# Kernel optimization log

Measured on AMD Instinct MI355X. Metric: run time of the kernel, lower is better.

## Reference

```python
import jax, jax.numpy as jnp
import numpy as np

B, S, D_MODEL, H, N_LAYERS = 4, 1024, 512, 8, 6
DEPTH = D_MODEL // H


def setup_inputs() -> dict:
    key = jax.random.key(0)
    ks = jax.random.split(key, 16)
    sc = 1.0 / np.sqrt(D_MODEL)
    inp = {
        'v': jax.random.normal(ks[0], (B, S, D_MODEL), jnp.float32),
        'q': jax.random.normal(ks[1], (B, S, D_MODEL), jnp.float32),
        'k': jax.random.normal(ks[2], (B, S, D_MODEL), jnp.float32),
        'wq_w': jax.random.normal(ks[3], (D_MODEL, D_MODEL), jnp.float32) * sc,
        'wq_b': jnp.zeros((D_MODEL,), jnp.float32),
        'wk_w': jax.random.normal(ks[4], (D_MODEL, D_MODEL), jnp.float32) * sc,
        'wk_b': jnp.zeros((D_MODEL,), jnp.float32),
        'wv_w': jax.random.normal(ks[5], (D_MODEL, D_MODEL), jnp.float32) * sc,
        'wv_b': jnp.zeros((D_MODEL,), jnp.float32),
        'wo_w': jax.random.normal(ks[6], (D_MODEL, D_MODEL), jnp.float32) * sc,
        'wo_b': jnp.zeros((D_MODEL,), jnp.float32),
        'aug_hb': jax.random.uniform(ks[7], (N_LAYERS, 1), jnp.float32),
        'aug_pi': jax.random.uniform(ks[8], (N_LAYERS, 1), jnp.float32),
        'aug_at': jax.random.uniform(ks[9], (N_LAYERS, 1), jnp.float32),
        'table_hb': jax.random.normal(ks[10], (S, S), jnp.float32),
        'table_pi': jax.random.normal(ks[11], (S, S), jnp.float32),
        'mask': (jax.random.uniform(ks[12], (B, 1, S, S)) < 0.1).astype(jnp.float32),
        'block_num': 0,
    }
    return inp


def _split_heads(x):
    # (B, S, d_model) -> (B, H, S, depth)
    return x.reshape(B, S, H, DEPTH).transpose(0, 2, 1, 3)


def reference(v, q, k, wq_w, wq_b, wk_w, wk_b, wv_w, wv_b, wo_w, wo_b,
              aug_hb, aug_pi, aug_at, table_hb, table_pi, mask, block_num):
    qh = _split_heads(q @ wq_w + wq_b)
    kh = _split_heads(k @ wk_w + wk_b)
    vh = _split_heads(v @ wv_w + wv_b)

    # NOTE: original call site swaps q/k positionally, so scores = K . Q^T
    scores = jnp.einsum('bhid,bhjd->bhij', kh, qh)  # (B,H,S,S)
    dk = jnp.float32(DEPTH)
    logits = scores / jnp.sqrt(dk) + mask * (-1e9)

    # per-layer table augmentation (tables broadcast over batch & heads)
    logits = logits * aug_at[block_num] \
        + aug_hb[block_num] * table_hb \
        + aug_pi[block_num] * table_pi

    # joint softmax over axes (2, 3)
    m = jnp.max(logits, axis=(2, 3), keepdims=True)
    e = jnp.exp(logits - m)
    attn = e / jnp.sum(e, axis=(2, 3), keepdims=True)

    ctx = jnp.einsum('bhij,bhjd->bhid', attn, vh)          # (B,H,S,depth)
    ctx = ctx.transpose(0, 2, 1, 3).reshape(B, S, D_MODEL)  # concat heads
    out = ctx @ wo_w + wo_b
    return out, attn
```

## Files before the change

kernel.cpp:

```cpp
#include <hip/hip_runtime.h>
#include <math.h>

#define NS 1024
#define DM 512
#define NH 8
#define DEPTH 64

#define OFF_QH   0
#define OFF_KH   2097152
#define OFF_VH   4194304
#define OFF_CTX0 0
#define OFF_CTX1 2097152
#define OFF_PART 6291456

#define SW3(row, col) ((col) ^ ((((row) >> 3) & 3) << 3))
#define ESW(row, col) ((col) ^ ((((row) >> 3) & 7) << 2))

#define LO_SCALE 2048.0f
#define LO_INV   (1.0f/2048.0f)
#define F16_MIN_NORM 6.1035156e-5f
#define ASCALE   4096.0f
#define AUNSCALE (1.0f/4096.0f)

typedef float f4 __attribute__((ext_vector_type(4)));
typedef _Float16 h8 __attribute__((ext_vector_type(8)));
typedef float f32x4v __attribute__((ext_vector_type(4)));

#define SPLIT1(x, hi_e, lo_e) {                                          \
    const float x_ = (x);                                                \
    _Float16 t = (fabsf(x_) >= F16_MIN_NORM) ? (_Float16)x_ : (_Float16)0.f; \
    hi_e = t;                                                            \
    lo_e = (_Float16)((x_ - (float)t) * LO_SCALE);                       \
}

#define SPLIT8(u0, u1, hi, lo) {                                         \
    SPLIT1(u0.x, hi[0], lo[0]) SPLIT1(u0.y, hi[1], lo[1])                \
    SPLIT1(u0.z, hi[2], lo[2]) SPLIT1(u0.w, hi[3], lo[3])                \
    SPLIT1(u1.x, hi[4], lo[4]) SPLIT1(u1.y, hi[5], lo[5])                \
    SPLIT1(u1.z, hi[6], lo[6]) SPLIT1(u1.w, hi[7], lo[7])                \
}

#define MM(accH, accM, a_h, a_l, b_h, b_l) {                                   \
    accH = __builtin_amdgcn_mfma_f32_16x16x32_f16(a_h, b_h, accH, 0, 0, 0);    \
    accM = __builtin_amdgcn_mfma_f32_16x16x32_f16(a_l, b_h, accM, 0, 0, 0);    \
    accM = __builtin_amdgcn_mfma_f32_16x16x32_f16(a_h, b_l, accM, 0, 0, 0);    \
}

__device__ __forceinline__ void prep_one(
    const float* __restrict__ W, _Float16* __restrict__ whi,
    _Float16* __restrict__ wlo, int g)
{
    const int kk = g >> 7;
    const int n  = (g & 127) * 4;
    const float4 f = *(const float4*)(W + (size_t)kk * DM + n);
    const int gbase = (kk >> 3) * 128 + (kk & 7);
    #define PREP1(val, nn) {                                             \
        const int a_ = ((nn) >> 4) * 8192 + gbase + ((nn) & 15) * 8;     \
        _Float16 h_; _Float16 l_;                                        \
        SPLIT1(val, h_, l_)                                              \
        whi[a_] = h_; wlo[a_] = l_;                                      \
    }
    PREP1(f.x, n + 0) PREP1(f.y, n + 1) PREP1(f.z, n + 2) PREP1(f.w, n + 3)
    #undef PREP1
}

__global__ __launch_bounds__(256) void k_prep_qkv(
    const float* __restrict__ wq, const float* __restrict__ wk,
    const float* __restrict__ wv, float* __restrict__ attn)
{
    const int w = blockIdx.y;
    const float* W = (w == 0) ? wq : (w == 1) ? wk : wv;
    _Float16* base = (_Float16*)attn + (size_t)w * 524288;
    prep_one(W, base, base + 262144, blockIdx.x * 256 + threadIdx.x);
}

__global__ __launch_bounds__(256) void k_prep_wo(
    const float* __restrict__ wo, float* __restrict__ ws)
{
    _Float16* base = (_Float16*)(ws + OFF_VH);
    prep_one(wo, base, base + 262144, blockIdx.x * 256 + threadIdx.x);
}

__global__ __launch_bounds__(256, 3) void k_proj(
    const float* __restrict__ q, const float* __restrict__ k, const float* __restrict__ v,
    const float* __restrict__ bq, const float* __restrict__ bk, const float* __restrict__ bv,
    float* __restrict__ ws, const float* __restrict__ attn)
{
    const float *X, *bias; float* out; int wsel;
    if (blockIdx.z == 0)      { X=q; bias=bq; out=ws+OFF_QH; wsel=0; }
    else if (blockIdx.z == 1) { X=k; bias=bk; out=ws+OFF_KH; wsel=1; }
    else                      { X=v; bias=bv; out=ws+OFF_VH; wsel=2; }

    const int f = blockIdx.x + (blockIdx.y << 3);
    const int n0 = (f >> 5) * 64, m0 = (f & 31) * 128;
    const int tid = threadIdx.x, l = tid & 63, w = tid >> 6;
    const int lr = l & 15, lg = l >> 4;

    const _Float16* whi = (const _Float16*)attn + (size_t)wsel * 524288;
    const _Float16* wlo = whi + 262144;
    const float* ap0 = X + (size_t)(m0 + w*32 + lr) * DM + lg*8;
    const float* ap1 = ap0 + (size_t)16 * DM;
    const _Float16* bh_base = whi + (size_t)(n0 >> 4) * 8192 + lg*128 + lr*8;
    const _Float16* bl_base = wlo + (size_t)(n0 >> 4) * 8192 + lg*128 + lr*8;

    f32x4v aH00 = 0, aH01 = 0, aH02 = 0, aH03 = 0;
    f32x4v aH10 = 0, aH11 = 0, aH12 = 0, aH13 = 0;
    f32x4v aM00 = 0, aM01 = 0, aM02 = 0, aM03 = 0;
    f32x4v aM10 = 0, aM11 = 0, aM12 = 0, aM13 = 0;

    #pragma unroll 1
    for (int kb = 0; kb < DM; kb += 32) {
        h8 ah0, al0, ah1, al1;
        {
            const float4 u0 = *(const float4*)(ap0 + kb);
            const float4 u1 = *(const float4*)(ap0 + kb + 4);
            SPLIT8(u0, u1, ah0, al0);
            const float4 v0 = *(const float4*)(ap1 + kb);
            const float4 v1 = *(const float4*)(ap1 + kb + 4);
            SPLIT8(v0, v1, ah1, al1);
        }
        const int boff = kb * 16;
        const h8 bh0 = *(const h8*)(bh_base + boff);
        const h8 bh1 = *(const h8*)(bh_base + boff + 8192);
        const h8 bh2 = *(const h8*)(bh_base + boff + 16384);
        const h8 bh3 = *(const h8*)(bh_base + boff + 24576);
        const h8 bl0 = *(const h8*)(bl_base + boff);
        const h8 bl1 = *(const h8*)(bl_base + boff + 8192);
        const h8 bl2 = *(const h8*)(bl_base + boff + 16384);
        const h8 bl3 = *(const h8*)(bl_base + boff + 24576);

        MM(aH00, aM00, ah0, al0, bh0, bl0) MM(aH01, aM01, ah0, al0, bh1, bl1)
        MM(aH02, aM02, ah0, al0, bh2, bl2) MM(aH03, aM03, ah0, al0, bh3, bl3)
        MM(aH10, aM10, ah1, al1, bh0, bl0) MM(aH11, aM11, ah1, al1, bh1, bl1)
        MM(aH12, aM12, ah1, al1, bh2, bl2) MM(aH13, aM13, ah1, al1, bh3, bl3)
    }

    const int h = n0 >> 6;
    #define STORE_TILE(accH, accM, nt, mt) {                                 \
        const int n = n0 + (nt)*16 + lr;                                     \
        const float bsv = bias[n];                                           \
        const int d = n & 63;                                                \
        const int mbase = m0 + w*32 + (mt)*16 + lg*4;                        \
        _Pragma("unroll")                                                    \
        for (int r = 0; r < 4; ++r) {                                        \
            const int m = mbase + r;                                         \
            const int bb = m >> 10, s = m & 1023;                            \
            out[(((size_t)(bb*NH + h))*NS + s)*DEPTH + d] =                  \
                fmaf(accM[r], LO_INV, accH[r]) + bsv;                        \
        }                                                                    \
    }
    STORE_TILE(aH00, aM00, 0, 0) STORE_TILE(aH10, aM10, 0, 1)
    STORE_TILE(aH01, aM01, 1, 0) STORE_TILE(aH11, aM11, 1, 1)
    STORE_TILE(aH02, aM02, 2, 0) STORE_TILE(aH12, aM12, 2, 1)
    STORE_TILE(aH03, aM03, 3, 0) STORE_TILE(aH13, aM13, 3, 1)
    #undef STORE_TILE
}

__global__ __launch_bounds__(256, 4) void k_sumexp(
    float* __restrict__ ws,
    const float* __restrict__ t_hb, const float* __restrict__ t_pi,
    const float* __restrict__ mask,
    const float* __restrict__ aug_hb, const float* __restrict__ aug_pi,
    const float* __restrict__ aug_at, const int* __restrict__ bnum,
    float* __restrict__ attn)
{
    __shared__ float Ks[32][132];
    __shared__ float Qs[32][132];
    __shared__ float wred[4];
    const int bh = blockIdx.z, b = bh >> 3;
    const int f = blockIdx.x + (blockIdx.y << 3);
    const int r = f & 7, qq = f >> 3;
    const int it = ((r & 1) << 2) | (qq & 3);
    const int jt = ((r >> 1) << 1) | (qq >> 2);
    const int i0 = it * 128, j0 = jt * 128;
    const float* kh = ws + OFF_KH + (size_t)bh*NS*DEPTH;
    const float* qh = ws + OFF_QH + (size_t)bh*NS*DEPTH;
    const int tid = threadIdx.x, tx = tid & 15, ty = tid >> 4;
    const int ar_ = tid >> 3, ac4 = tid & 7;

    float acc[8][8] = {};
    for (int d0 = 0; d0 < DEPTH; d0 += 32) {
        #pragma unroll
        for (int l = 0; l < 4; ++l) {
            const int rr = ar_ + l*32;
            const float4 fk = *(const float4*)(kh + (size_t)(i0+rr)*DEPTH + d0 + ac4*4);
            Ks[ac4*4+0][SW3(ac4*4+0, rr)]=fk.x; Ks[ac4*4+1][SW3(ac4*4+1, rr)]=fk.y;
            Ks[ac4*4+2][SW3(ac4*4+2, rr)]=fk.z; Ks[ac4*4+3][SW3(ac4*4+3, rr)]=fk.w;
            const float4 fq = *(const float4*)(qh + (size_t)(j0+rr)*DEPTH + d0 + ac4*4);
            Qs[ac4*4+0][SW3(ac4*4+0, rr)]=fq.x; Qs[ac4*4+1][SW3(ac4*4+1, rr)]=fq.y;
            Qs[ac4*4+2][SW3(ac4*4+2, rr)]=fq.z; Qs[ac4*4+3][SW3(ac4*4+3, rr)]=fq.w;
        }
        __syncthreads();
        #pragma unroll
        for (int d = 0; d < 32; ++d) {
            const float4 fa0 = *(const float4*)&Ks[d][SW3(d, ty*4)];
            const float4 fa1 = *(const float4*)&Ks[d][SW3(d, 64+ty*4)];
            const float4 fb0 = *(const float4*)&Qs[d][SW3(d, tx*4)];
            const float4 fb1 = *(const float4*)&Qs[d][SW3(d, 64+tx*4)];
            const float av[8] = {fa0.x,fa0.y,fa0.z,fa0.w,fa1.x,fa1.y,fa1.z,fa1.w};
            const float bw[8] = {fb0.x,fb0.y,fb0.z,fb0.w,fb1.x,fb1.y,fb1.z,fb1.w};
            #pragma unroll
            for (int i = 0; i < 8; ++i)
                #pragma unroll
                for (int j = 0; j < 8; ++j)
                    acc[i][j] = fmaf(av[i], bw[j], acc[i][j]);
        }
        __syncthreads();
    }

    const int bn = bnum[0];
    const float at = aug_at[bn], hb = aug_hb[bn], pi = aug_pi[bn];
    const float sc_at = 0.125f*at, m_at = -1e9f*at;
    float local = 0.f;
    #pragma unroll
    for (int i = 0; i < 8; ++i) {
        const int gi = i0 + (i>>2)*64 + ty*4 + (i&3);
        const size_t mrow = ((size_t)b*NS + gi)*NS;
        const size_t trow = (size_t)gi*NS;
        const size_t arow = ((size_t)bh*NS + gi)*NS;
        #pragma unroll
        for (int cb = 0; cb < 2; ++cb) {
            const int gj = j0 + cb*64 + tx*4;
            const float4 m4 = *(const float4*)(mask + mrow + gj);
            const float4 h4 = *(const float4*)(t_hb + trow + gj);
            const float4 p4 = *(const float4*)(t_pi + trow + gj);
            f4 e4;
            e4.x = __expf(fmaf(acc[i][cb*4+0], sc_at, fmaf(m4.x, m_at, fmaf(hb, h4.x, pi*p4.x))));
            e4.y = __expf(fmaf(acc[i][cb*4+1], sc_at, fmaf(m4.y, m_at, fmaf(hb, h4.y, pi*p4.y))));
            e4.z = __expf(fmaf(acc[i][cb*4+2], sc_at, fmaf(m4.z, m_at, fmaf(hb, h4.z, pi*p4.z))));
            e4.w = __expf(fmaf(acc[i][cb*4+3], sc_at, fmaf(m4.w, m_at, fmaf(hb, h4.w, pi*p4.w))));
            __builtin_nontemporal_store(e4, (f4*)(attn + arow + gj));
            local += (e4.x + e4.y) + (e4.z + e4.w);
        }
    }
    #pragma unroll
    for (int o = 32; o > 0; o >>= 1) local += __shfl_down(local, o);
    if ((tid & 63) == 0) wred[tid >> 6] = local;
    __syncthreads();
    if (tid == 0)
        ws[OFF_PART + bh*64 + it*8 + jt] =
            (wred[0] + wred[1]) + (wred[2] + wred[3]);
}

__global__ __launch_bounds__(256, 4) void k_pv(
    float* __restrict__ ws, float* __restrict__ attn)
{
    __shared__ float Es[64][68];
    __shared__ float Vs[64][68];
    __shared__ float s_inv;
    const int F = blockIdx.x + (blockIdx.y << 1) + (blockIdx.z << 5);
    const int r = F & 7, s = F >> 3;
    const int bh = (r << 2) | (s & 3);
    const int w = s >> 2;
    const int i0 = (w >> 1) * 64;
    const int jh = w & 1;
    const int b = bh >> 3, h = bh & 7;
    const float* vh = ws + OFF_VH + (size_t)bh*NS*DEPTH;
    float* pctx = ws + (jh ? OFF_CTX1 : OFF_CTX0);
    const int tid = threadIdx.x, tx = tid & 15, ty = tid >> 4;
    const int er_ = tid >> 4, ec4 = tid & 15;

    if (tid < 64) {
        float vsum = ws[OFF_PART + bh*64 + tid];
        #pragma unroll
        for (int o = 32; o > 0; o >>= 1) vsum += __shfl_down(vsum, o);
        if (tid == 0) s_inv = 1.0f / vsum;
    }
    __syncthreads();
    const float inv = s_inv;

    float acc[4][4] = {};
    for (int jt = 0; jt < 8; ++jt) {
        const int j0 = jh*512 + jt*64;
        #pragma unroll
        for (int l = 0; l < 4; ++l) {
            const int rr = er_ + l*16;
            float* ap = attn + ((size_t)bh*NS + i0 + rr)*NS + j0 + ec4*4;
            f4 e4 = __builtin_nontemporal_load((const f4*)ap);
            e4 *= inv;
            __builtin_nontemporal_store(e4, (f4*)ap);
            Es[ec4*4+0][ESW(ec4*4+0, rr)] = e4.x;
            Es[ec4*4+1][ESW(ec4*4+1, rr)] = e4.y;
            Es[ec4*4+2][ESW(ec4*4+2, rr)] = e4.z;
            Es[ec4*4+3][ESW(ec4*4+3, rr)] = e4.w;
            *(float4*)&Vs[rr][ec4*4] = *(const float4*)(vh + (size_t)(j0+rr)*DEPTH + ec4*4);
        }
        __syncthreads();
        #pragma unroll
        for (int jj = 0; jj < 64; ++jj) {
            const float4 a  = *(const float4*)&Es[jj][ESW(jj, ty*4)];
            const float4 vv = *(const float4*)&Vs[jj][tx*4];
            const float av[4] = {a.x,a.y,a.z,a.w};
            const float vw[4] = {vv.x,vv.y,vv.z,vv.w};
            #pragma unroll
            for (int i = 0; i < 4; ++i)
                #pragma unroll
                for (int d = 0; d < 4; ++d)
                    acc[i][d] = fmaf(av[i], vw[d], acc[i][d]);
        }
        __syncthreads();
    }
    #pragma unroll
    for (int i = 0; i < 4; ++i) {
        const int gi = i0 + ty*4 + i;
        float4 o;
        o.x = acc[i][0]; o.y = acc[i][1]; o.z = acc[i][2]; o.w = acc[i][3];
        *(float4*)(pctx + ((size_t)b*NS + gi)*DM + h*DEPTH + tx*4) = o;
    }
}

__global__ __launch_bounds__(256, 3) void k_out(
    const float* __restrict__ wsc, const float* __restrict__ bo,
    float* __restrict__ outp)
{
    const int f = blockIdx.x + (blockIdx.y << 3);
    const int n0 = (f >> 5) * 64, m0 = (f & 31) * 128;
    const int tid = threadIdx.x, l = tid & 63, w = tid >> 6;
    const int lr = l & 15, lg = l >> 4;

    const _Float16* whi = (const _Float16*)(wsc + OFF_VH);
    const _Float16* wlo = whi + 262144;
    const float* ap0 = wsc + OFF_CTX0 + (size_t)(m0 + w*32 + lr) * DM + lg*8;
    const float* ap1 = wsc + OFF_CTX1 + (size_t)(m0 + w*32 + lr) * DM + lg*8;
    const _Float16* bh_base = whi + (size_t)(n0 >> 4) * 8192 + lg*128 + lr*8;
    const _Float16* bl_base = wlo + (size_t)(n0 >> 4) * 8192 + lg*128 + lr*8;

    f32x4v aH00 = 0, aH01 = 0, aH02 = 0, aH03 = 0;
    f32x4v aH10 = 0, aH11 = 0, aH12 = 0, aH13 = 0;
    f32x4v aM00 = 0, aM01 = 0, aM02 = 0, aM03 = 0;
    f32x4v aM10 = 0, aM11 = 0, aM12 = 0, aM13 = 0;

    #pragma unroll 1
    for (int kb = 0; kb < DM; kb += 32) {
        h8 ah0, al0, ah1, al1;
        {
            float4 u0 = *(const float4*)(ap0 + kb);
            float4 u1 = *(const float4*)(ap0 + kb + 4);
            const float4 c0 = *(const float4*)(ap1 + kb);
            const float4 c1 = *(const float4*)(ap1 + kb + 4);
            u0.x=(u0.x+c0.x)*ASCALE; u0.y=(u0.y+c0.y)*ASCALE;
            u0.z=(u0.z+c0.z)*ASCALE; u0.w=(u0.w+c0.w)*ASCALE;
            u1.x=(u1.x+c1.x)*ASCALE; u1.y=(u1.y+c1.y)*ASCALE;
            u1.z=(u1.z+c1.z)*ASCALE; u1.w=(u1.w+c1.w)*ASCALE;
            SPLIT8(u0, u1, ah0, al0);
            float4 v0 = *(const float4*)(ap0 + (size_t)16*DM + kb);
            float4 v1 = *(const float4*)(ap0 + (size_t)16*DM + kb + 4);
            const float4 d0 = *(const float4*)(ap1 + (size_t)16*DM + kb);
            const float4 d1 = *(const float4*)(ap1 + (size_t)16*DM + kb + 4);
            v0.x=(v0.x+d0.x)*ASCALE; v0.y=(v0.y+d0.y)*ASCALE;
            v0.z=(v0.z+d0.z)*ASCALE; v0.w=(v0.w+d0.w)*ASCALE;
            v1.x=(v1.x+d1.x)*ASCALE; v1.y=(v1.y+d1.y)*ASCALE;
            v1.z=(v1.z+d1.z)*ASCALE; v1.w=(v1.w+d1.w)*ASCALE;
            SPLIT8(v0, v1, ah1, al1);
        }
        const int boff = kb * 16;
        const h8 bh0 = *(const h8*)(bh_base + boff);
        const h8 bh1 = *(const h8*)(bh_base + boff + 8192);
        const h8 bh2 = *(const h8*)(bh_base + boff + 16384);
        const h8 bh3 = *(const h8*)(bh_base + boff + 24576);
        const h8 bl0 = *(const h8*)(bl_base + boff);
        const h8 bl1 = *(const h8*)(bl_base + boff + 8192);
        const h8 bl2 = *(const h8*)(bl_base + boff + 16384);
        const h8 bl3 = *(const h8*)(bl_base + boff + 24576);

        MM(aH00, aM00, ah0, al0, bh0, bl0) MM(aH01, aM01, ah0, al0, bh1, bl1)
        MM(aH02, aM02, ah0, al0, bh2, bl2) MM(aH03, aM03, ah0, al0, bh3, bl3)
        MM(aH10, aM10, ah1, al1, bh0, bl0) MM(aH11, aM11, ah1, al1, bh1, bl1)
        MM(aH12, aM12, ah1, al1, bh2, bl2) MM(aH13, aM13, ah1, al1, bh3, bl3)
    }

    #define STORE_TILE(accH, accM, nt, mt) {                                 \
        const int n = n0 + (nt)*16 + lr;                                     \
        const float bsv = bo[n];                                             \
        const int mbase = m0 + w*32 + (mt)*16 + lg*4;                        \
        _Pragma("unroll")                                                    \
        for (int r = 0; r < 4; ++r)                                          \
            outp[(size_t)(mbase + r)*DM + n] =                               \
                fmaf(accM[r], LO_INV, accH[r]) * AUNSCALE + bsv;             \
    }
    STORE_TILE(aH00, aM00, 0, 0) STORE_TILE(aH10, aM10, 0, 1)
    STORE_TILE(aH01, aM01, 1, 0) STORE_TILE(aH11, aM11, 1, 1)
    STORE_TILE(aH02, aM02, 2, 0) STORE_TILE(aH12, aM12, 2, 1)
    STORE_TILE(aH03, aM03, 3, 0) STORE_TILE(aH13, aM13, 3, 1)
    #undef STORE_TILE
}

extern "C" void kernel_launch(void* const* d_in, const int* in_sizes, int n_in,
                              void* d_out, int out_size, void* d_ws, size_t ws_size,
                              hipStream_t stream)
{
    const float* v    = (const float*)d_in[0];
    const float* q    = (const float*)d_in[1];
    const float* k    = (const float*)d_in[2];
    const float* wq_w = (const float*)d_in[3];
    const float* wq_b = (const float*)d_in[4];
    const float* wk_w = (const float*)d_in[5];
    const float* wk_b = (const float*)d_in[6];
    const float* wv_w = (const float*)d_in[7];
    const float* wv_b = (const float*)d_in[8];
    const float* wo_w = (const float*)d_in[9];
    const float* wo_b = (const float*)d_in[10];
    const float* aug_hb = (const float*)d_in[11];
    const float* aug_pi = (const float*)d_in[12];
    const float* aug_at = (const float*)d_in[13];
    const float* t_hb   = (const float*)d_in[14];
    const float* t_pi   = (const float*)d_in[15];
    const float* mask   = (const float*)d_in[16];
    const int*   bnum   = (const int*)d_in[17];

    float* ws   = (float*)d_ws;
    float* outp = (float*)d_out;
    float* attn = (float*)d_out + (size_t)4*NS*DM;

    hipLaunchKernelGGL(k_prep_qkv, dim3(256, 3), dim3(256), 0, stream,
                       wq_w, wk_w, wv_w, attn);
    hipLaunchKernelGGL(k_proj, dim3(8, 32, 3), dim3(256), 0, stream,
                       q, k, v, wq_b, wk_b, wv_b, ws, attn);
    hipLaunchKernelGGL(k_sumexp, dim3(8, 8, 32), dim3(256), 0, stream,
                       ws, t_hb, t_pi, mask, aug_hb, aug_pi, aug_at, bnum, attn);
    hipLaunchKernelGGL(k_pv, dim3(2, 16, 32), dim3(256), 0, stream, ws, attn);
    hipLaunchKernelGGL(k_prep_wo, dim3(256, 1), dim3(256), 0, stream, wo_w, ws);
    hipLaunchKernelGGL(k_out, dim3(8, 32), dim3(256), 0, stream,
                       ws, wo_b, outp);
}
```

Baseline: 259.8 us.

## Compute attention scores with split-fp16 MFMA instead of fp32 FMA tiles

```diff
diff --git a/kernel.cpp b/kernel.cpp
--- a/kernel.cpp
+++ b/kernel.cpp
@@ -13,7 +13,6 @@
 #define OFF_CTX1 2097152
 #define OFF_PART 6291456
 
-#define SW3(row, col) ((col) ^ ((((row) >> 3) & 3) << 3))
 #define ESW(row, col) ((col) ^ ((((row) >> 3) & 7) << 2))
 
 #define LO_SCALE 2048.0f
@@ -44,6 +43,11 @@
     accH = __builtin_amdgcn_mfma_f32_16x16x32_f16(a_h, b_h, accH, 0, 0, 0);    \
     accM = __builtin_amdgcn_mfma_f32_16x16x32_f16(a_l, b_h, accM, 0, 0, 0);    \
     accM = __builtin_amdgcn_mfma_f32_16x16x32_f16(a_h, b_l, accM, 0, 0, 0);    \
+}
+#define MM1(acc, a_h, a_l, b_h, b_l) {                                         \
+    acc = __builtin_amdgcn_mfma_f32_16x16x32_f16(a_h, b_h, acc, 0, 0, 0);      \
+    acc = __builtin_amdgcn_mfma_f32_16x16x32_f16(a_l, b_h, acc, 0, 0, 0);      \
+    acc = __builtin_amdgcn_mfma_f32_16x16x32_f16(a_h, b_l, acc, 0, 0, 0);      \
 }
 
 __device__ __forceinline__ void prep_one(
@@ -86,10 +90,12 @@
     const float* __restrict__ bq, const float* __restrict__ bk, const float* __restrict__ bv,
     float* __restrict__ ws, const float* __restrict__ attn)
 {
-    const float *X, *bias; float* out; int wsel;
-    if (blockIdx.z == 0)      { X=q; bias=bq; out=ws+OFF_QH; wsel=0; }
-    else if (blockIdx.z == 1) { X=k; bias=bk; out=ws+OFF_KH; wsel=1; }
-    else                      { X=v; bias=bv; out=ws+OFF_VH; wsel=2; }
+    const float *X, *bias; int wsel;
+    if (blockIdx.z == 0)      { X=q; bias=bq; wsel=0; }
+    else if (blockIdx.z == 1) { X=k; bias=bk; wsel=1; }
+    else                      { X=v; bias=bv; wsel=2; }
+    float* outf = ws + OFF_VH;
+    _Float16* outh = (_Float16*)(ws + (wsel == 0 ? OFF_QH : OFF_KH));
 
     const int f = blockIdx.x + (blockIdx.y << 3);
     const int n0 = (f >> 5) * 64, m0 = (f & 31) * 128;
@@ -145,8 +151,16 @@
         for (int r = 0; r < 4; ++r) {                                        \
             const int m = mbase + r;                                         \
             const int bb = m >> 10, s = m & 1023;                            \
-            out[(((size_t)(bb*NH + h))*NS + s)*DEPTH + d] =                  \
-                fmaf(accM[r], LO_INV, accH[r]) + bsv;                        \
+            const float val = fmaf(accM[r], LO_INV, accH[r]) + bsv;          \
+            if (wsel == 2) {                                                 \
+                outf[(((size_t)(bb*NH + h))*NS + s)*DEPTH + d] = val;        \
+            } else {                                                         \
+                _Float16* p = outh + (size_t)(bb*NH + h)*131072              \
+                                   + (size_t)s*64 + d;                       \
+                const _Float16 hi_ = (_Float16)val;                          \
+                p[0]     = hi_;                                              \
+                p[65536] = (_Float16)(val - (float)hi_);                     \
+            }                                                                \
         }                                                                    \
     }
     STORE_TILE(aH00, aM00, 0, 0) STORE_TILE(aH10, aM10, 0, 1)
@@ -156,7 +170,7 @@
     #undef STORE_TILE
 }
 
-__global__ __launch_bounds__(256, 4) void k_sumexp(
+__global__ __launch_bounds__(256, 3) void k_score(
     float* __restrict__ ws,
     const float* __restrict__ t_hb, const float* __restrict__ t_pi,
     const float* __restrict__ mask,
@@ -164,48 +178,36 @@
     const float* __restrict__ aug_at, const int* __restrict__ bnum,
     float* __restrict__ attn)
 {
-    __shared__ float Ks[32][132];
-    __shared__ float Qs[32][132];
     __shared__ float wred[4];
     const int bh = blockIdx.z, b = bh >> 3;
     const int f = blockIdx.x + (blockIdx.y << 3);
     const int r = f & 7, qq = f >> 3;
     const int it = ((r & 1) << 2) | (qq & 3);
-    const int jt = ((r >> 1) << 1) | (qq >> 2);
-    const int i0 = it * 128, j0 = jt * 128;
-    const float* kh = ws + OFF_KH + (size_t)bh*NS*DEPTH;
-    const float* qh = ws + OFF_QH + (size_t)bh*NS*DEPTH;
-    const int tid = threadIdx.x, tx = tid & 15, ty = tid >> 4;
-    const int ar_ = tid >> 3, ac4 = tid & 7;
-
-    float acc[8][8] = {};
-    for (int d0 = 0; d0 < DEPTH; d0 += 32) {
+    const int jt_ = ((r >> 1) << 1) | (qq >> 2);
+    const int i0 = it * 128, j0 = jt_ * 128;
+    const _Float16* kb_ = (const _Float16*)(ws + OFF_KH) + (size_t)bh * 131072;
+    const _Float16* qb_ = (const _Float16*)(ws + OFF_QH) + (size_t)bh * 131072;
+    const int tid = threadIdx.x, l = tid & 63, w = tid >> 6;
+    const int lr = l & 15, lg = l >> 4;
+
+    const _Float16* ka = kb_ + (size_t)(i0 + w*32 + lr) * 64 + lg*8;
+    const _Float16* qa = qb_ + (size_t)(j0 + lr) * 64 + lg*8;
+
+    f32x4v acc[2][8] = {};
+    #pragma unroll
+    for (int d0 = 0; d0 < 2; ++d0) {
+        const int dd = d0 * 32;
+        const h8 ah0 = *(const h8*)(ka + dd);
+        const h8 al0 = *(const h8*)(ka + dd + 65536);
+        const h8 ah1 = *(const h8*)(ka + dd + 16*64);
+        const h8 al1 = *(const h8*)(ka + dd + 16*64 + 65536);
         #pragma unroll
-        for (int l = 0; l < 4; ++l) {
-            const int rr = ar_ + l*32;
-            const float4 fk = *(const float4*)(kh + (size_t)(i0+rr)*DEPTH + d0 + ac4*4);
-            Ks[ac4*4+0][SW3(ac4*4+0, rr)]=fk.x; Ks[ac4*4+1][SW3(ac4*4+1, rr)]=fk.y;
-            Ks[ac4*4+2][SW3(ac4*4+2, rr)]=fk.z; Ks[ac4*4+3][SW3(ac4*4+3, rr)]=fk.w;
-            const float4 fq = *(const float4*)(qh + (size_t)(j0+rr)*DEPTH + d0 + ac4*4);
-            Qs[ac4*4+0][SW3(ac4*4+0, rr)]=fq.x; Qs[ac4*4+1][SW3(ac4*4+1, rr)]=fq.y;
-            Qs[ac4*4+2][SW3(ac4*4+2, rr)]=fq.z; Qs[ac4*4+3][SW3(ac4*4+3, rr)]=fq.w;
-        }
-        __syncthreads();
-        #pragma unroll
-        for (int d = 0; d < 32; ++d) {
-            const float4 fa0 = *(const float4*)&Ks[d][SW3(d, ty*4)];
-            const float4 fa1 = *(const float4*)&Ks[d][SW3(d, 64+ty*4)];
-            const float4 fb0 = *(const float4*)&Qs[d][SW3(d, tx*4)];
-            const float4 fb1 = *(const float4*)&Qs[d][SW3(d, 64+tx*4)];
-            const float av[8] = {fa0.x,fa0.y,fa0.z,fa0.w,fa1.x,fa1.y,fa1.z,fa1.w};
-            const float bw[8] = {fb0.x,fb0.y,fb0.z,fb0.w,fb1.x,fb1.y,fb1.z,fb1.w};
-            #pragma unroll
-            for (int i = 0; i < 8; ++i)
-                #pragma unroll
-                for (int j = 0; j < 8; ++j)
-                    acc[i][j] = fmaf(av[i], bw[j], acc[i][j]);
-        }
-        __syncthreads();
+        for (int jt = 0; jt < 8; ++jt) {
+            const h8 bhf = *(const h8*)(qa + dd + jt*16*64);
+            const h8 blf = *(const h8*)(qa + dd + jt*16*64 + 65536);
+            MM1(acc[0][jt], ah0, al0, bhf, blf)
+            MM1(acc[1][jt], ah1, al1, bhf, blf)
+        }
     }
 
     const int bn = bnum[0];
@@ -213,24 +215,24 @@
     const float sc_at = 0.125f*at, m_at = -1e9f*at;
     float local = 0.f;
     #pragma unroll
-    for (int i = 0; i < 8; ++i) {
-        const int gi = i0 + (i>>2)*64 + ty*4 + (i&3);
-        const size_t mrow = ((size_t)b*NS + gi)*NS;
-        const size_t trow = (size_t)gi*NS;
-        const size_t arow = ((size_t)bh*NS + gi)*NS;
+    for (int it2 = 0; it2 < 2; ++it2) {
         #pragma unroll
-        for (int cb = 0; cb < 2; ++cb) {
-            const int gj = j0 + cb*64 + tx*4;
-            const float4 m4 = *(const float4*)(mask + mrow + gj);
-            const float4 h4 = *(const float4*)(t_hb + trow + gj);
-            const float4 p4 = *(const float4*)(t_pi + trow + gj);
-            f4 e4;
-            e4.x = __expf(fmaf(acc[i][cb*4+0], sc_at, fmaf(m4.x, m_at, fmaf(hb, h4.x, pi*p4.x))));
-            e4.y = __expf(fmaf(acc[i][cb*4+1], sc_at, fmaf(m4.y, m_at, fmaf(hb, h4.y, pi*p4.y))));
-            e4.z = __expf(fmaf(acc[i][cb*4+2], sc_at, fmaf(m4.z, m_at, fmaf(hb, h4.z, pi*p4.z))));
-            e4.w = __expf(fmaf(acc[i][cb*4+3], sc_at, fmaf(m4.w, m_at, fmaf(hb, h4.w, pi*p4.w))));
-            __builtin_nontemporal_store(e4, (f4*)(attn + arow + gj));
-            local += (e4.x + e4.y) + (e4.z + e4.w);
+        for (int rr = 0; rr < 4; ++rr) {
+            const int gi = i0 + w*32 + it2*16 + lg*4 + rr;
+            const size_t mrow = ((size_t)b*NS + gi)*NS;
+            const size_t trow = (size_t)gi*NS;
+            const size_t arow = ((size_t)bh*NS + gi)*NS;
+            #pragma unroll
+            for (int jt = 0; jt < 8; ++jt) {
+                const int gj = j0 + jt*16 + lr;
+                const float mv = mask[mrow + gj];
+                const float th = t_hb[trow + gj];
+                const float tp = t_pi[trow + gj];
+                const float e = __expf(fmaf(acc[it2][jt][rr], sc_at,
+                                       fmaf(mv, m_at, fmaf(hb, th, pi*tp))));
+                __builtin_nontemporal_store(e, attn + arow + gj);
+                local += e;
+            }
         }
     }
     #pragma unroll
@@ -238,7 +240,7 @@
     if ((tid & 63) == 0) wred[tid >> 6] = local;
     __syncthreads();
     if (tid == 0)
-        ws[OFF_PART + bh*64 + it*8 + jt] =
+        ws[OFF_PART + bh*64 + it*8 + jt_] =
             (wred[0] + wred[1]) + (wred[2] + wred[3]);
 }
 
@@ -416,7 +418,7 @@
                        wq_w, wk_w, wv_w, attn);
     hipLaunchKernelGGL(k_proj, dim3(8, 32, 3), dim3(256), 0, stream,
                        q, k, v, wq_b, wk_b, wv_b, ws, attn);
-    hipLaunchKernelGGL(k_sumexp, dim3(8, 8, 32), dim3(256), 0, stream,
+    hipLaunchKernelGGL(k_score, dim3(8, 8, 32), dim3(256), 0, stream,
                        ws, t_hb, t_pi, mask, aug_hb, aug_pi, aug_at, bnum, attn);
     hipLaunchKernelGGL(k_pv, dim3(2, 16, 32), dim3(256), 0, stream, ws, attn);
     hipLaunchKernelGGL(k_prep_wo, dim3(256, 1), dim3(256), 0, stream, wo_w, ws);
```

Measured after the change: 242.9 us. 1.07x faster.
